# Optimization experiments

Hardware: AMD Instinct MI355X
Metric: run time of the kernel (lower is better)

## Reference

```python
import jax, jax.numpy as jnp
import numpy as np


def _kb_beta(kw, osf):
    # Beatty Kaiser-Bessel shape parameter used by gpuNUFFT
    return float(np.pi * np.sqrt((kw / osf) ** 2 * (osf - 0.5) ** 2 - 0.8))


def _deapod_1d(img_dim, grid_dim, kw, beta):
    # Inverse FT of the KB kernel evaluated on the image grid (deapodization).
    u = (np.arange(img_dim) - img_dim / 2.0) / grid_dim
    z = np.sqrt((np.pi * kw * u) ** 2 - beta ** 2 + 0j)
    a = np.real(np.sin(z) / z)  # sin->sinh automatically via complex sqrt
    return a.astype(np.float32)


def setup_inputs() -> dict:
    key = jax.random.key(0)
    k0, k1, k2, k3 = jax.random.split(key, 4)
    H = 320
    C = 16
    M = 204800
    x = jax.random.normal(k0, (H, H, 2), dtype=jnp.float32)
    csm = jax.random.normal(k1, (C, H, H, 2), dtype=jnp.float32) / jnp.sqrt(float(C))
    trajectory = jax.random.uniform(k2, (2, M), dtype=jnp.float32, minval=-0.5, maxval=0.5)
    dcf = jax.random.uniform(k3, (M,), dtype=jnp.float32, minval=0.01, maxval=1.0)
    return {"x": x, "csm": csm, "trajectory": trajectory, "dcf": dcf,
            "img_dim": 320, "osf": 2, "kernel_width": 3}


def reference(x, csm, trajectory, dcf, img_dim, osf, kernel_width):
    kw = int(kernel_width)
    G = int(osf) * int(img_dim)
    beta = _kb_beta(kw, osf)
    half = kw // 2

    xc = x[..., 0] + 1j * x[..., 1]            # [H,W] complex
    cc = csm[..., 0] + 1j * csm[..., 1]        # [C,H,W] complex

    # 1) coil images + deapodization
    a1 = _deapod_1d(img_dim, G, kw, beta)
    apod = jnp.asarray(np.outer(a1, a1))       # [H,W]
    img = cc * xc[None] / apod[None]           # [C,H,W]

    # 2) zero-pad to oversampled grid, centered FFT
    pad = (G - int(img_dim)) // 2
    C = cc.shape[0]
    grid = jnp.zeros((C, G, G), dtype=img.dtype).at[:, pad:pad + int(img_dim), pad:pad + int(img_dim)].set(img)
    ksp = jnp.fft.fftshift(
        jnp.fft.fft2(jnp.fft.ifftshift(grid, axes=(-2, -1)), axes=(-2, -1)),
        axes=(-2, -1)) / G

    # 3) Kaiser-Bessel interpolation (degridding) at non-uniform points
    p = trajectory * G + G / 2.0               # [2,M] grid coords
    ctr = jnp.rint(p)

    def kb(d):
        t = 1.0 - (2.0 * d / kw) ** 2
        return jnp.where(t > 0, jnp.i0(beta * jnp.sqrt(jnp.maximum(t, 0.0))), 0.0) / kw

    acc = jnp.zeros((C, p.shape[1]), dtype=ksp.dtype)
    for oy in range(-half, half + 1):
        ny = ctr[0] + oy
        wy = kb(ny - p[0])
        iy = jnp.mod(ny, G).astype(jnp.int32)
        for ox in range(-half, half + 1):
            nx = ctr[1] + ox
            wx = kb(nx - p[1])
            ix = jnp.mod(nx, G).astype(jnp.int32)
            acc = acc + ksp[:, iy, ix] * (wy * wx)[None].astype(ksp.dtype)

    # 4) density compensation (sqrt weighting, as in optox gpuNUFFT wrapper)
    y = acc * jnp.sqrt(dcf)[None].astype(acc.dtype)
    return jnp.stack([jnp.real(y), jnp.imag(y)], axis=-1)  # [C,M,2] float32
```

## Files before the change

kernel.cpp:

```cpp
#include <hip/hip_runtime.h>
#include <hip/hip_fp16.h>

#define PI_F      3.14159265358979323846f
#define TWO_PI_F  6.28318530717958647692f
#define BETA      6.4860766f
#define NM        204800
#define NBIN      1600
#define BCAP      256
#define CPAD      16
#define HALO      18
#define HSTRIDE   9
#define TS16      649

__device__ __forceinline__ float2 cmulf(float2 a, float2 b){
    return make_float2(a.x*b.x - a.y*b.y, a.x*b.y + a.y*b.x);
}

__device__ __forceinline__ float i0_dev(float x){
    if (x < 3.75f){
        float t = x * (1.0f/3.75f); t *= t;
        return 1.0f + t*(3.5156229f + t*(3.0899424f + t*(1.2067492f +
                     t*(0.2659732f + t*(0.0360768f + t*0.0045813f)))));
    } else {
        float u = 3.75f / x;
        float p = 0.39894228f + u*(0.01328592f + u*(0.00225319f + u*(-0.00157565f +
                  u*(0.00916281f + u*(-0.02057706f + u*(0.02635537f +
                  u*(-0.01647633f + u*0.00392377f)))))));
        return p * expf(x) * rsqrtf(x);
    }
}

__device__ __forceinline__ float kbw(float d){
    float dd = d * (2.0f/3.0f);
    float t = 1.0f - dd*dd;
    if (t <= 0.0f) return 0.0f;
    return i0_dev(BETA * sqrtf(t)) * (1.0f/3.0f);
}

__device__ __forceinline__ int bin_of(float py, float px){
    int yy = (int)rintf(py); yy %= 640; if (yy < 0) yy += 640;
    int xx = (int)rintf(px); xx %= 640; if (xx < 0) xx += 640;
    return (yy >> 4) * 40 + (xx >> 4);
}

__global__ __launch_bounds__(1024) void k_init(float2* __restrict__ tw,
                                               float* __restrict__ ia1,
                                               int* __restrict__ counts){
    int tid = threadIdx.x;
    int g = blockIdx.x*1024 + tid;
    if (g < NBIN*CPAD) counts[g] = 0;
    if (blockIdx.x == 0){
        if (tid < 640){
            float sn, cs; sincosf((float)tid * (-TWO_PI_F/640.0f), &sn, &cs);
            tw[tid] = make_float2(cs, sn);
        }
        if (tid < 320){
            float u = (tid - 160.0f) * (1.0f/640.0f);
            float v = 3.0f * PI_F * u;
            float q = v*v - BETA*BETA;
            float a;
            if (q >= 0.0f){
                float z = sqrtf(q);
                a = (z > 1e-20f) ? (sinf(z)/z) : 1.0f;
            } else {
                float s = sqrtf(-q);
                a = (expf(s) - expf(-s)) / (2.0f*s);
            }
            ia1[tid] = 1.0f / (a * 25.298221281347036f);
        }
    }
}

__device__ __forceinline__ void fft640_wave(float2 r[10],
                                            const float2* __restrict__ tw,
                                            int a){
    const float c5r[5] = {1.0f, 0.30901699f, -0.80901699f, -0.80901699f, 0.30901699f};
    const float c5i[5] = {0.0f, -0.95105652f, -0.58778525f, 0.58778525f, 0.95105652f};
    float2 v0[5], v1[5];
    const int i0[5] = {0,2,4,6,8};
    const int i1[5] = {5,7,9,1,3};
    #pragma unroll
    for (int k2=0;k2<5;k2++){
        float ax=r[i0[0]].x, ay=r[i0[0]].y, bx=r[i1[0]].x, by=r[i1[0]].y;
        #pragma unroll
        for (int n2=1;n2<5;n2++){
            const int jj = (n2*k2)%5;
            ax += r[i0[n2]].x*c5r[jj] - r[i0[n2]].y*c5i[jj];
            ay += r[i0[n2]].x*c5i[jj] + r[i0[n2]].y*c5r[jj];
            bx += r[i1[n2]].x*c5r[jj] - r[i1[n2]].y*c5i[jj];
            by += r[i1[n2]].x*c5i[jj] + r[i1[n2]].y*c5r[jj];
        }
        v0[k2]=make_float2(ax,ay); v1[k2]=make_float2(bx,by);
    }
    float2 y[10];
    const int o0[5] = {0,6,2,8,4};
    const int o1[5] = {5,1,7,3,9};
    #pragma unroll
    for (int k2=0;k2<5;k2++){
        y[o0[k2]] = make_float2(v0[k2].x+v1[k2].x, v0[k2].y+v1[k2].y);
        y[o1[k2]] = make_float2(v0[k2].x-v1[k2].x, v0[k2].y-v1[k2].y);
    }
    float2 w1 = tw[a]; w1.x = -w1.x; w1.y = -w1.y;
    float2 w = w1;
    r[0] = y[0];
    #pragma unroll
    for (int q=1;q<10;q++){
        r[q] = cmulf(y[q], w);
        if (q < 9) w = cmulf(w, w1);
    }
    float2 ws = tw[5*a];
    #pragma unroll
    for (int h=32; h>=1; h>>=1){
        ws = cmulf(ws, ws);
        bool up = (a & h) != 0;
        if (up){ ws.x = -ws.x; ws.y = -ws.y; }
        #pragma unroll
        for (int q=0;q<10;q++){
            float px = __shfl_xor(r[q].x, h);
            float py = __shfl_xor(r[q].y, h);
            if (!up){ r[q].x += px; r[q].y += py; }
            else      r[q] = cmulf(make_float2(px - r[q].x, py - r[q].y), ws);
        }
    }
}

__global__ __launch_bounds__(1024) void k_fft1s(const float2* __restrict__ x,
                                                const float2* __restrict__ csm,
                                                const float* __restrict__ ia1,
                                                const float2* __restrict__ tw,
                                                const float* __restrict__ traj,
                                                const float* __restrict__ dcf,
                                                int* __restrict__ counts,
                                                float4* __restrict__ st,
                                                __half2* __restrict__ staged,
                                                __half2* __restrict__ bufB){
    __shared__ __half2 tile[16][TS16];
    int b = blockIdx.x;
    if (b >= 320){
        int m = (b - 320)*1024 + threadIdx.x;
        float py = traj[m]      * 640.0f + 320.0f;
        float px = traj[NM + m] * 640.0f + 320.0f;
        int bi = bin_of(py, px);
        int pos = atomicAdd(&counts[bi*CPAD], 1);
        if (pos < BCAP){
            st[bi*BCAP + pos] = make_float4(py, px, sqrtf(dcf[m]), __int_as_float(m));
        } else {
            __half2 z = __floats2half2_rn(0.0f, 0.0f);
            __half2* o = staged + (size_t)m*16;
            #pragma unroll
            for (int c=0;c<16;c++) o[c] = z;
        }
        return;
    }
    int c  = b / 20;
    int y0 = (b - c*20) * 16;
    int tid = threadIdx.x;
    int w = tid >> 6;
    int a = tid & 63;
    int y = y0 + w;
    float iay = ia1[y];
    float2 r[10];
    #pragma unroll
    for (int j=0;j<10;j++){
        int n = a + 64*j;
        float2 v = make_float2(0.0f, 0.0f);
        if (n >= 160 && n < 480){
            int xi = n - 160;
            int rr = y*320 + xi;
            float2 xv = x[rr];
            float2 cv = csm[c*102400 + rr];
            float scl = iay * ia1[xi];
            if ((y + xi) & 1) scl = -scl;
            v.x = (cv.x*xv.x - cv.y*xv.y) * scl;
            v.y = (cv.x*xv.y + cv.y*xv.x) * scl;
        }
        r[j] = v;
    }
    fft640_wave(r, tw, a);
    int kbase = 10 * (__brev((unsigned)a) >> 26);
    #pragma unroll
    for (int q=0;q<10;q++) tile[w][kbase + q] = __floats2half2_rn(r[q].x, r[q].y);
    __syncthreads();
    for (int idx = tid; idx < 16*640; idx += 1024){
        int kx = idx >> 4;
        int f  = idx & 15;
        bufB[(c*640 + kx)*320 + (y0 + f)] = tile[f][kx];
    }
}

__global__ __launch_bounds__(1024) void k_fft2(const __half2* __restrict__ bufB,
                                               const float2* __restrict__ tw,
                                               __half2* __restrict__ kspH){
    __shared__ __half2 tile[16][TS16];
    int kx = blockIdx.x;
    int tid = threadIdx.x;
    int w = tid >> 6;
    int a = tid & 63;
    const __half2* src = bufB + ((size_t)w*640 + kx)*320;
    float2 r[10];
    #pragma unroll
    for (int j=0;j<10;j++){
        int n = a + 64*j;
        float2 v = make_float2(0.0f, 0.0f);
        if (n >= 160 && n < 480){
            __half2 hv = src[n - 160];
            v = make_float2(__low2float(hv), __high2float(hv));
        }
        r[j] = v;
    }
    fft640_wave(r, tw, a);
    int kbase = 10 * (__brev((unsigned)a) >> 26);
    #pragma unroll
    for (int q=0;q<10;q++) tile[w][kbase + q] = __floats2half2_rn(r[q].x, r[q].y);
    __syncthreads();
    for (int idx = tid; idx < 16*640; idx += 1024){
        int ky = idx >> 4;
        int c  = idx & 15;
        kspH[((size_t)kx*640 + ky)*16 + c] = tile[c][ky];
    }
}

__global__ __launch_bounds__(256) void k_interp3(const int* __restrict__ counts,
                                                 const float4* __restrict__ st,
                                                 const __half2* __restrict__ kspH,
                                                 __half2* __restrict__ staged){
    __shared__ float4 hal[HALO*HALO*HSTRIDE];
    int b = blockIdx.x;
    int ns = counts[b*CPAD];
    if (ns > BCAP) ns = BCAP;
    if (ns == 0) return;
    int s0 = b * BCAP;
    int by16 = (b / 40) * 16;
    int bx16 = (b - (b/40)*40) * 16;
    int tid = threadIdx.x;
    for (int i = tid; i < HALO*HALO*4; i += 256){
        int q  = i & 3;
        int pt = i >> 2;
        int rr = pt % HALO;
        int j  = pt / HALO;
        int gy = by16 - 1 + rr; if (gy < 0) gy += 640; if (gy >= 640) gy -= 640;
        int gx = bx16 - 1 + j;  if (gx < 0) gx += 640; if (gx >= 640) gx -= 640;
        float4 raw = ((const float4*)(kspH + ((size_t)gx*640 + gy)*16))[q];
        const __half2* hp = (const __half2*)&raw;
        int base = (rr*HALO + j)*HSTRIDE + q*2;
        hal[base]     = make_float4(__low2float(hp[0]), __high2float(hp[0]),
                                    __low2float(hp[1]), __high2float(hp[1]));
        hal[base + 1] = make_float4(__low2float(hp[2]), __high2float(hp[2]),
                                    __low2float(hp[3]), __high2float(hp[3]));
    }
    __syncthreads();
    for (int u = tid; u < 2*ns; u += 256){
        int s = u >> 1;
        int h = u & 1;
        float4 s4 = st[s0 + s];
        float py = s4.x, px = s4.y, sc = s4.z;
        int m = __float_as_int(s4.w);
        float cy = rintf(py), cx = rintf(px);
        float d0 = h ? (cx - px) : (cy - py);
        float wa[3], wb[3];
        #pragma unroll
        for (int j=0;j<3;j++) wa[j] = kbw(d0 + (float)(j-1));
        #pragma unroll
        for (int j=0;j<3;j++) wb[j] = __shfl_xor(wa[j], 1);
        float wy[3], wx[3];
        #pragma unroll
        for (int j=0;j<3;j++){
            wy[j] = h ? wb[j] : wa[j];
            wx[j] = h ? wa[j] : wb[j];
        }
        int ry[3], rx[3];
        #pragma unroll
        for (int j=0;j<3;j++){
            int yy = (int)cy + (j-1) - (by16 - 1);
            if (yy < 0) yy += 640; if (yy >= 640) yy -= 640;
            ry[j] = yy;
            int xx = (int)cx + (j-1) - (bx16 - 1);
            if (xx < 0) xx += 640; if (xx >= 640) xx -= 640;
            rx[j] = xx;
        }
        float2 acc[8];
        #pragma unroll
        for (int c=0;c<8;c++) acc[c] = make_float2(0.0f, 0.0f);
        #pragma unroll
        for (int jy=0;jy<3;jy++){
            #pragma unroll
            for (int jx=0;jx<3;jx++){
                float w = wy[jy]*wx[jx];
                const float4* p = &hal[(ry[jy]*HALO + rx[jx])*HSTRIDE + h*4];
                #pragma unroll
                for (int q=0;q<4;q++){
                    float4 v = p[q];
                    acc[2*q].x   = fmaf(w, v.x, acc[2*q].x);
                    acc[2*q].y   = fmaf(w, v.y, acc[2*q].y);
                    acc[2*q+1].x = fmaf(w, v.z, acc[2*q+1].x);
                    acc[2*q+1].y = fmaf(w, v.w, acc[2*q+1].y);
                }
            }
        }
        __half2* o = staged + (size_t)m*16 + h*8;
        #pragma unroll
        for (int c=0;c<8;c++)
            o[c] = __floats2half2_rn(acc[c].x*sc, acc[c].y*sc);
    }
}

__global__ __launch_bounds__(256) void k_unperm(const __half2* __restrict__ staged,
                                                float2* __restrict__ out){
    int m = blockIdx.x*256 + threadIdx.x;
    const float4* p4 = (const float4*)(staged + (size_t)m*16);
    #pragma unroll
    for (int q=0;q<4;q++){
        float4 raw = p4[q];
        const __half2* hp = (const __half2*)&raw;
        #pragma unroll
        for (int k=0;k<4;k++)
            out[(4*q + k)*NM + m] = make_float2(__low2float(hp[k]), __high2float(hp[k]));
    }
}

extern "C" void kernel_launch(void* const* d_in, const int* in_sizes, int n_in,
                              void* d_out, int out_size, void* d_ws, size_t ws_size,
                              hipStream_t stream) {
    (void)in_sizes; (void)n_in; (void)out_size; (void)ws_size;
    const float* x    = (const float*)d_in[0];
    const float* csm  = (const float*)d_in[1];
    const float* traj = (const float*)d_in[2];
    const float* dcf  = (const float*)d_in[3];
    float* out = (float*)d_out;

    char* ws = (char*)d_ws;
    float2*  tw     = (float2*)ws;
    float*   ia1    = (float*)(ws + 8192);
    int*     counts = (int*)(ws + 16384);
    float4*  st     = (float4*)(ws + 1048576);
    __half2* kspH   = (__half2*)(ws + 8388608);
    __half2* bufB   = (__half2*)(ws + 8388608 + 26214400ull);
    __half2* staged = (__half2*)(ws + 8388608 + 26214400ull + 13107200ull);

    k_init   <<<26, 1024, 0, stream>>>(tw, ia1, counts);
    k_fft1s  <<<520, 1024, 0, stream>>>((const float2*)x, (const float2*)csm, ia1, tw,
                                        traj, dcf, counts, st, staged, bufB);
    k_fft2   <<<640, 1024, 0, stream>>>(bufB, tw, kspH);
    k_interp3<<<NBIN, 256, 0, stream>>>(counts, st, kspH, staged);
    k_unperm <<<800, 256, 0, stream>>>(staged, (float2*)out);
}
```

Measured before the change: 81.52 us.

## Store interp halo as half2 in LDS and use polynomial KB weights

The interpolation kernel now keeps the halo tile in shared memory as packed half2 instead of expanded float4. This halves the LDS footprint and store traffic, at the cost of half-to-float conversions in the inner loop. The Bessel-based KB weight is replaced by a single 12th-degree polynomial in (1-d^2·4/9), which removes branches and the exp and rsqrt calls. Each thread now computes all six weights itself rather than sharing them through a lane shuffle, trading extra ALU work for less cross-lane communication.

Result: faster. 74.58 us (-8.5%).

```diff
diff --git a/kernel.cpp b/kernel.cpp
--- a/kernel.cpp
+++ b/kernel.cpp
@@ -9,32 +9,29 @@
 #define BCAP      256
 #define CPAD      16
 #define HALO      18
-#define HSTRIDE   9
+#define HP2S      20
 #define TS16      649
 
 __device__ __forceinline__ float2 cmulf(float2 a, float2 b){
     return make_float2(a.x*b.x - a.y*b.y, a.x*b.y + a.y*b.x);
 }
 
-__device__ __forceinline__ float i0_dev(float x){
-    if (x < 3.75f){
-        float t = x * (1.0f/3.75f); t *= t;
-        return 1.0f + t*(3.5156229f + t*(3.0899424f + t*(1.2067492f +
-                     t*(0.2659732f + t*(0.0360768f + t*0.0045813f)))));
-    } else {
-        float u = 3.75f / x;
-        float p = 0.39894228f + u*(0.01328592f + u*(0.00225319f + u*(-0.00157565f +
-                  u*(0.00916281f + u*(-0.02057706f + u*(0.02635537f +
-                  u*(-0.01647633f + u*0.00392377f)))))));
-        return p * expf(x) * rsqrtf(x);
-    }
-}
-
 __device__ __forceinline__ float kbw(float d){
-    float dd = d * (2.0f/3.0f);
-    float t = 1.0f - dd*dd;
-    if (t <= 0.0f) return 0.0f;
-    return i0_dev(BETA * sqrtf(t)) * (1.0f/3.0f);
+    float v = 1.0f - d*d*(4.0f/9.0f);
+    float p = 7.983104e-6f;
+    p = fmaf(p, v, 1.0930295e-4f);
+    p = fmaf(p, v, 1.2575152e-3f);
+    p = fmaf(p, v, 1.1956629e-2f);
+    p = fmaf(p, v, 9.2085150e-2f);
+    p = fmaf(p, v, 5.6035800e-1f);
+    p = fmaf(p, v, 2.6107030f);
+    p = fmaf(p, v, 8.9362880f);
+    p = fmaf(p, v, 21.241972f);
+    p = fmaf(p, v, 32.315456f);
+    p = fmaf(p, v, 27.653388f);
+    p = fmaf(p, v, 10.517297f);
+    p = fmaf(p, v, 1.0f);
+    return (v > 0.0f) ? p * (1.0f/3.0f) : 0.0f;
 }
 
 __device__ __forceinline__ int bin_of(float py, float px){
@@ -224,7 +221,7 @@
                                                  const float4* __restrict__ st,
                                                  const __half2* __restrict__ kspH,
                                                  __half2* __restrict__ staged){
-    __shared__ float4 hal[HALO*HALO*HSTRIDE];
+    __shared__ __half2 hal[HALO*HALO*HP2S];
     int b = blockIdx.x;
     int ns = counts[b*CPAD];
     if (ns > BCAP) ns = BCAP;
@@ -241,12 +238,7 @@
         int gy = by16 - 1 + rr; if (gy < 0) gy += 640; if (gy >= 640) gy -= 640;
         int gx = bx16 - 1 + j;  if (gx < 0) gx += 640; if (gx >= 640) gx -= 640;
         float4 raw = ((const float4*)(kspH + ((size_t)gx*640 + gy)*16))[q];
-        const __half2* hp = (const __half2*)&raw;
-        int base = (rr*HALO + j)*HSTRIDE + q*2;
-        hal[base]     = make_float4(__low2float(hp[0]), __high2float(hp[0]),
-                                    __low2float(hp[1]), __high2float(hp[1]));
-        hal[base + 1] = make_float4(__low2float(hp[2]), __high2float(hp[2]),
-                                    __low2float(hp[3]), __high2float(hp[3]));
+        *(float4*)&hal[(rr*HALO + j)*HP2S + q*4] = raw;
     }
     __syncthreads();
     for (int u = tid; u < 2*ns; u += 256){
@@ -256,21 +248,13 @@
         float py = s4.x, px = s4.y, sc = s4.z;
         int m = __float_as_int(s4.w);
         float cy = rintf(py), cx = rintf(px);
-        float d0 = h ? (cx - px) : (cy - py);
-        float wa[3], wb[3];
-        #pragma unroll
-        for (int j=0;j<3;j++) wa[j] = kbw(d0 + (float)(j-1));
-        #pragma unroll
-        for (int j=0;j<3;j++) wb[j] = __shfl_xor(wa[j], 1);
         float wy[3], wx[3];
+        int ry[3], rx[3];
         #pragma unroll
         for (int j=0;j<3;j++){
-            wy[j] = h ? wb[j] : wa[j];
-            wx[j] = h ? wa[j] : wb[j];
-        }
-        int ry[3], rx[3];
-        #pragma unroll
-        for (int j=0;j<3;j++){
+            float o = (float)(j-1);
+            wy[j] = kbw(cy + o - py);
+            wx[j] = kbw(cx + o - px);
             int yy = (int)cy + (j-1) - (by16 - 1);
             if (yy < 0) yy += 640; if (yy >= 640) yy -= 640;
             ry[j] = yy;
@@ -286,14 +270,19 @@
             #pragma unroll
             for (int jx=0;jx<3;jx++){
                 float w = wy[jy]*wx[jx];
-                const float4* p = &hal[(ry[jy]*HALO + rx[jx])*HSTRIDE + h*4];
+                const __half2* p = &hal[(ry[jy]*HALO + rx[jx])*HP2S + h*8];
+                float4 rawA = *(const float4*)(p);
+                float4 rawB = *(const float4*)(p + 4);
+                const __half2* ha = (const __half2*)&rawA;
+                const __half2* hb = (const __half2*)&rawB;
                 #pragma unroll
                 for (int q=0;q<4;q++){
-                    float4 v = p[q];
-                    acc[2*q].x   = fmaf(w, v.x, acc[2*q].x);
-                    acc[2*q].y   = fmaf(w, v.y, acc[2*q].y);
-                    acc[2*q+1].x = fmaf(w, v.z, acc[2*q+1].x);
-                    acc[2*q+1].y = fmaf(w, v.w, acc[2*q+1].y);
+                    float2 va = __half22float2(ha[q]);
+                    acc[q].x = fmaf(w, va.x, acc[q].x);
+                    acc[q].y = fmaf(w, va.y, acc[q].y);
+                    float2 vb = __half22float2(hb[q]);
+                    acc[4+q].x = fmaf(w, vb.x, acc[4+q].x);
+                    acc[4+q].y = fmaf(w, vb.y, acc[4+q].y);
                 }
             }
         }
```
